# Performance work log

Measured on AMD Instinct MI355X. Metric: run time of the kernel, lower is better.

The kernel has to match this reference:

```python
import jax, jax.numpy as jnp
import numpy as np
import math

N, L, D = 1024, 32, 768
N_OUT, IN_DIM, OUT_DIM = 16, 64, 64
EPS = 1e-8


def setup_inputs() -> dict:
    key = jax.random.key(0)
    ks = jax.random.split(key, 4)
    x = jax.random.normal(ks[0], (N, L, D), jnp.float32)
    mask = jnp.ones((N, L), jnp.float32)
    scaled = lambda k, shape, fan: jax.random.normal(k, shape, jnp.float32) * (1.0 / np.sqrt(fan).astype(np.float32))
    Wscore = scaled(ks[1], (L, D, 1), D)
    Bscore = jnp.zeros((L, 1, 1), jnp.float32)
    Wcap = scaled(ks[2], (L, D, IN_DIM), D)
    Bcap = jnp.zeros((L, 1, IN_DIM), jnp.float32)
    Wvote = scaled(ks[3], (L, N_OUT, IN_DIM, OUT_DIM), IN_DIM)
    Bvote = jnp.zeros((L, N_OUT, 1, OUT_DIM), jnp.float32)
    beta_use = jnp.zeros((L, 1, 1, 1), jnp.float32)
    beta_ign = jnp.zeros((1, N_OUT, 1, 1), jnp.float32)
    return dict(x=x, mask=mask, Wscore=Wscore, Bscore=Bscore, Wcap=Wcap,
                Bcap=Bcap, Wvote=Wvote, Bvote=Bvote, beta_use=beta_use,
                beta_ign=beta_ign, iters=3)


def reference(x, mask, Wscore, Bscore, Wcap, Bcap, Wvote, Bvote, beta_use, beta_ign, iters):
    n_out = Wvote.shape[1]
    half_pi = np.float32(0.5 * math.pi)
    x_t = jnp.transpose(x, (1, 0, 2))                      # [L, N, D]
    a_in = jnp.matmul(x_t, Wscore) + Bscore                # [L, N, 1]
    mu_in = jax.nn.gelu(jnp.matmul(x_t, Wcap) + Bcap, approximate=False)  # [L, N, in_dim]
    f_a_in = jax.nn.sigmoid(a_in) * jnp.transpose(mask)[..., None]        # [L, N, 1]
    f_a_in = f_a_in[:, None, :, :]                         # [L, 1, N, 1]
    # votes: [L, n_out, N, out_dim] (einsum avoids materializing repeated mu_in)
    V = jnp.einsum('lni,lkio->lkno', mu_in, Wvote) + Bvote

    R = jnp.full((1, n_out, 1, 1), 1.0 / n_out, dtype=x.dtype)
    a_out = mu_out = var_out = None
    for t in range(iters):
        if t > 0:
            log_p = (-jnp.sum((V - mu_out[None]) ** 2 / (2.0 * var_out[None] + EPS), axis=-1)
                     - 1.0 - half_pi
                     - 0.5 * jnp.sum(jnp.log(var_out[None] + EPS), axis=-1))   # [L, n_out, N]
            R = jax.nn.softmax(jax.nn.log_sigmoid(a_out)[None] + log_p[..., None], axis=1)
        D_use = f_a_in * R                                  # [L, n_out, N, 1]
        D_ign = f_a_in - D_use
        a_out = jnp.sum(beta_use * D_use, axis=0) - jnp.sum(beta_ign * D_ign, axis=0)  # [n_out, N, 1]
        denom = jnp.sum(D_use, axis=0) + EPS                # [n_out, N, 1]
        mu_out = jnp.sum(D_use * V, axis=0) / denom         # [n_out, N, out_dim]
        var_out = jnp.sum(D_use * (V - mu_out[None]) ** 2, axis=0) / denom

    a_fin = jnp.transpose(a_out[..., 0])                    # [N, n_out]
    mu_fin = jnp.transpose(mu_out, (1, 0, 2))               # [N, n_out, out_dim]
    return a_fin, mu_fin
```

## Files before the change

### kernel.cpp

```cpp
#include <hip/hip_runtime.h>
#include <hip/hip_bf16.h>

#define L_DIM 32
#define N_DIM 1024
#define D_DIM 768
#define K_DIM 16
#define I_DIM 64
#define O_DIM 64
#define EPSF 1e-8f
#define PX 72

typedef unsigned short u16;
typedef __attribute__((ext_vector_type(8))) short short8;
typedef __attribute__((ext_vector_type(4))) float f32x4;
#define MFMA __builtin_amdgcn_mfma_f32_16x16x32_bf16

__device__ __forceinline__ float bf2f(u16 v) {
    union { unsigned int u; float f; } x; x.u = ((unsigned int)v) << 16; return x.f;
}
__device__ __forceinline__ u16 f2bf(float f) {
    union { float f; unsigned int u; } x; x.f = f;
    unsigned int u = x.u;
    u += 0x7FFFu + ((u >> 16) & 1u);
    return (u16)(u >> 16);
}
__device__ __forceinline__ void split2(float v, u16& h, u16& l) {
    u16 hh = f2bf(v);
    h = hh;
    l = f2bf(v - bf2f(hh));
}
__device__ __forceinline__ void store_split4(u16* ph, u16* pl, float4 v) {
    unsigned u0 = __float_as_uint(v.x), u1 = __float_as_uint(v.y);
    unsigned u2 = __float_as_uint(v.z), u3 = __float_as_uint(v.w);
    uint2 H, L;
    H.x = (u0 >> 16) | (u1 & 0xFFFF0000u);
    H.y = (u2 >> 16) | (u3 & 0xFFFF0000u);
    float l0 = v.x - __uint_as_float(u0 & 0xFFFF0000u);
    float l1 = v.y - __uint_as_float(u1 & 0xFFFF0000u);
    float l2 = v.z - __uint_as_float(u2 & 0xFFFF0000u);
    float l3 = v.w - __uint_as_float(u3 & 0xFFFF0000u);
    L.x = (__float_as_uint(l0) >> 16) | (__float_as_uint(l1) & 0xFFFF0000u);
    L.y = (__float_as_uint(l2) >> 16) | (__float_as_uint(l3) & 0xFFFF0000u);
    *(uint2*)ph = H;
    *(uint2*)pl = L;
}

__global__ __launch_bounds__(256) void prep_wcap(
    const float* __restrict__ W, u16* __restrict__ H, u16* __restrict__ Lo)
{
    const int l = blockIdx.y, d0 = blockIdx.x * 64, t = threadIdx.x;
    __shared__ float tile[64][65];
    #pragma unroll
    for (int p = 0; p < 4; p++) {
        int dd = p * 16 + (t >> 4), i4 = (t & 15) * 4;
        float4 v = *(const float4*)&W[((size_t)l * D_DIM + d0 + dd) * I_DIM + i4];
        tile[dd][i4] = v.x; tile[dd][i4+1] = v.y; tile[dd][i4+2] = v.z; tile[dd][i4+3] = v.w;
    }
    __syncthreads();
    #pragma unroll
    for (int p = 0; p < 4; p++) {
        int i = p * 16 + (t >> 4), dd0 = (t & 15) * 4;
        u16 h[4], lo[4];
        #pragma unroll
        for (int j = 0; j < 4; j++) split2(tile[dd0 + j][i], h[j], lo[j]);
        size_t base = ((size_t)l * I_DIM + i) * D_DIM + d0 + dd0;
        uint2 ph; ph.x = h[0] | ((unsigned)h[1] << 16); ph.y = h[2] | ((unsigned)h[3] << 16);
        uint2 pl; pl.x = lo[0] | ((unsigned)lo[1] << 16); pl.y = lo[2] | ((unsigned)lo[3] << 16);
        *(uint2*)&H[base] = ph;
        *(uint2*)&Lo[base] = pl;
    }
}

__global__ __launch_bounds__(256) void prep_wvote(
    const float* __restrict__ W, u16* __restrict__ H, u16* __restrict__ Lo)
{
    const int l = blockIdx.y, k = blockIdx.x, t = threadIdx.x;
    __shared__ float tile[64][65];
    #pragma unroll
    for (int p = 0; p < 4; p++) {
        int i = p * 16 + (t >> 4), o4 = (t & 15) * 4;
        float4 v = *(const float4*)&W[(((size_t)l * K_DIM + k) * I_DIM + i) * O_DIM + o4];
        tile[i][o4] = v.x; tile[i][o4+1] = v.y; tile[i][o4+2] = v.z; tile[i][o4+3] = v.w;
    }
    __syncthreads();
    #pragma unroll
    for (int p = 0; p < 4; p++) {
        int o = p * 16 + (t >> 4), i0 = (t & 15) * 4;
        u16 h[4], lo[4];
        #pragma unroll
        for (int j = 0; j < 4; j++) split2(tile[i0 + j][o], h[j], lo[j]);
        size_t base = (((size_t)l * K_DIM + k) * O_DIM + o) * I_DIM + i0;
        uint2 ph; ph.x = h[0] | ((unsigned)h[1] << 16); ph.y = h[2] | ((unsigned)h[3] << 16);
        uint2 pl; pl.x = lo[0] | ((unsigned)lo[1] << 16); pl.y = lo[2] | ((unsigned)lo[3] << 16);
        *(uint2*)&H[base] = ph;
        *(uint2*)&Lo[base] = pl;
    }
}

__global__ __launch_bounds__(256) void kernelA(
    const float* __restrict__ x, const float* __restrict__ mask,
    const float* __restrict__ Wscore, const float* __restrict__ Bscore,
    const u16* __restrict__ WcH, const u16* __restrict__ WcL,
    const float* __restrict__ Bcap,
    float* __restrict__ mu_out, float* __restrict__ fa_out,
    int nbase, int nchunk)
{
    const int l   = blockIdx.y;
    const int n0l = blockIdx.x * 32;
    const int t    = threadIdx.x;
    const int w    = t >> 6;
    const int lane = t & 63;
    const int quad = lane >> 4;
    const int ln16 = lane & 15;

    __shared__ u16 xh[2][32][PX], xl[2][32][PX];
    __shared__ float wsc_s[D_DIM];
    __shared__ float bcap_s[64];

    for (int i = t; i < D_DIM; i += 256) wsc_s[i] = Wscore[l * D_DIM + i];
    if (t < 64) bcap_s[t] = Bcap[l * I_DIM + t];

    const int sg = t >> 4;
    const int sd = (t & 15) * 4;

    const size_t xoff0 = ((size_t)(nbase + n0l + sg) * L_DIM + l) * D_DIM;
    const size_t xoff1 = ((size_t)(nbase + n0l + 16 + sg) * L_DIM + l) * D_DIM;

    float4 r0 = *(const float4*)&x[xoff0 + sd];
    float4 r1 = *(const float4*)&x[xoff1 + sd];

    __syncthreads();

    f32x4 acc[2] = {{0.f,0.f,0.f,0.f},{0.f,0.f,0.f,0.f}};
    float fa0 = 0.f, fa1 = 0.f;

    for (int ch = 0; ch < 12; ch++) {
        const int buf = ch & 1;
        const int k0 = ch * 64;

        {
            const float* wp = &wsc_s[k0 + sd];
            fa0 += r0.x * wp[0] + r0.y * wp[1] + r0.z * wp[2] + r0.w * wp[3];
            fa1 += r1.x * wp[0] + r1.y * wp[1] + r1.z * wp[2] + r1.w * wp[3];
        }
        store_split4(&xh[buf][sg][sd],      &xl[buf][sg][sd],      r0);
        store_split4(&xh[buf][16 + sg][sd], &xl[buf][16 + sg][sd], r1);
        __syncthreads();

        if (ch + 1 < 12) {
            const int k1 = k0 + 64;
            r0 = *(const float4*)&x[xoff0 + k1 + sd];
            r1 = *(const float4*)&x[xoff1 + k1 + sd];
        }

        #pragma unroll
        for (int ks = 0; ks < 2; ks++) {
            const int kk = ks * 32;
            size_t wbase = ((size_t)l * I_DIM + (w * 16 + ln16)) * D_DIM + k0 + kk + quad * 8;
            short8 ah = *(const short8*)&WcH[wbase];
            short8 al = *(const short8*)&WcL[wbase];
            #pragma unroll
            for (int c = 0; c < 2; c++) {
                const int n = c * 16 + ln16;
                short8 bh = *(const short8*)&xh[buf][n][kk + quad * 8];
                short8 bl = *(const short8*)&xl[buf][n][kk + quad * 8];
                acc[c] = MFMA(ah, bh, acc[c], 0, 0, 0);
                acc[c] = MFMA(ah, bl, acc[c], 0, 0, 0);
                acc[c] = MFMA(al, bh, acc[c], 0, 0, 0);
            }
        }
    }

    fa0 += __shfl_xor(fa0, 1, 64); fa1 += __shfl_xor(fa1, 1, 64);
    fa0 += __shfl_xor(fa0, 2, 64); fa1 += __shfl_xor(fa1, 2, 64);
    fa0 += __shfl_xor(fa0, 4, 64); fa1 += __shfl_xor(fa1, 4, 64);
    fa0 += __shfl_xor(fa0, 8, 64); fa1 += __shfl_xor(fa1, 8, 64);
    if ((t & 15) == 0) {
        float bs = Bscore[l];
        {
            float a = fa0 + bs;
            float sig = 1.f / (1.f + expf(-a));
            float m = mask[(size_t)(nbase + n0l + sg) * L_DIM + l];
            fa_out[(size_t)l * nchunk + n0l + sg] = sig * m;
        }
        {
            float a = fa1 + bs;
            float sig = 1.f / (1.f + expf(-a));
            float m = mask[(size_t)(nbase + n0l + 16 + sg) * L_DIM + l];
            fa_out[(size_t)l * nchunk + n0l + 16 + sg] = sig * m;
        }
    }

    #pragma unroll
    for (int c = 0; c < 2; c++) {
        const int n = c * 16 + ln16;
        const int i0 = w * 16 + quad * 4;
        float4 o;
        float* op = (float*)&o;
        #pragma unroll
        for (int r = 0; r < 4; r++) {
            float v = acc[c][r] + bcap_s[i0 + r];
            op[r] = 0.5f * v * (1.f + erff(v * 0.70710678118f));
        }
        *(float4*)&mu_out[((size_t)l * nchunk + n0l + n) * I_DIM + i0] = o;
    }
}

__global__ __launch_bounds__(256) void kernelB(
    const float* __restrict__ mu_in,
    const u16* __restrict__ WvH, const u16* __restrict__ WvL,
    const float* __restrict__ Bvote,
    float* __restrict__ V, int nchunk)
{
    const int l   = blockIdx.z;
    const int k   = blockIdx.y;
    const int n0l = blockIdx.x * 64;
    const int t    = threadIdx.x;
    const int w    = t >> 6;
    const int lane = t & 63;
    const int quad = lane >> 4;
    const int ln16 = lane & 15;

    __shared__ u16 mh[64][PX], ml[64][PX];
    __shared__ float bvote_s[64];

    if (t < 64) bvote_s[t] = Bvote[((size_t)l * K_DIM + k) * O_DIM + t];

    #pragma unroll
    for (int p = 0; p < 4; p++) {
        int n = p * 16 + (t >> 4), i0 = (t & 15) * 4;
        float4 v = *(const float4*)&mu_in[((size_t)l * nchunk + n0l + n) * I_DIM + i0];
        store_split4(&mh[n][i0], &ml[n][i0], v);
    }
    __syncthreads();

    f32x4 acc[4] = {{0.f,0.f,0.f,0.f},{0.f,0.f,0.f,0.f},{0.f,0.f,0.f,0.f},{0.f,0.f,0.f,0.f}};

    #pragma unroll
    for (int ks = 0; ks < 2; ks++) {
        const int kk = ks * 32;
        size_t wbase = (((size_t)l * K_DIM + k) * O_DIM + (w * 16 + ln16)) * I_DIM + kk + quad * 8;
        short8 ah = *(const short8*)&WvH[wbase];
        short8 al = *(const short8*)&WvL[wbase];
        #pragma unroll
        for (int c = 0; c < 4; c++) {
            const int n = c * 16 + ln16;
            short8 bh = *(const short8*)&mh[n][kk + quad * 8];
            short8 bl = *(const short8*)&ml[n][kk + quad * 8];
            acc[c] = MFMA(ah, bh, acc[c], 0, 0, 0);
            acc[c] = MFMA(ah, bl, acc[c], 0, 0, 0);
            acc[c] = MFMA(al, bh, acc[c], 0, 0, 0);
        }
    }

    #pragma unroll
    for (int c = 0; c < 4; c++) {
        const int n = c * 16 + ln16;
        const int o0 = w * 16 + quad * 4;
        float4 o;
        o.x = acc[c][0] + bvote_s[o0];
        o.y = acc[c][1] + bvote_s[o0 + 1];
        o.z = acc[c][2] + bvote_s[o0 + 2];
        o.w = acc[c][3] + bvote_s[o0 + 3];
        *(float4*)&V[(((size_t)l * K_DIM + k) * nchunk + n0l + n) * O_DIM + o0] = o;
    }
}

__global__ __launch_bounds__(256) void kernelC(
    const float* __restrict__ V, const float* __restrict__ fa_in,
    const float* __restrict__ beta_use, const float* __restrict__ beta_ign,
    const int* __restrict__ iters_p,
    float* __restrict__ out, int nbase, int nchunk)
{
    const int nl = blockIdx.x;
    const int ng = nbase + nl;
    const int t  = threadIdx.x;
    const int k  = t >> 4;
    const int og = (t & 15) << 2;
    int iters = iters_p[0];
    if (iters < 0 || iters > 16) iters = 3;

    __shared__ float fa_s[32];
    __shared__ float bu_s[32];
    __shared__ float R_s[32][17];
    __shared__ float sc_s[32][17];

    if (t < 32) {
        fa_s[t] = fa_in[(size_t)t * nchunk + nl];
        bu_s[t] = beta_use[t];
    }
    for (int idx = t; idx < 512; idx += 256)
        R_s[idx >> 4][idx & 15] = 1.f / 16.f;
    const float bi_k = beta_ign[k];

    float Vr[32][4];
    #pragma unroll
    for (int l = 0; l < 32; l++) {
        float4 v = *(const float4*)&V[(((size_t)l * K_DIM + k) * nchunk + nl) * O_DIM + og];
        Vr[l][0] = v.x; Vr[l][1] = v.y; Vr[l][2] = v.z; Vr[l][3] = v.w;
    }
    __syncthreads();

    float mu_r[4] = {0.f, 0.f, 0.f, 0.f};
    float var_r[4] = {0.f, 0.f, 0.f, 0.f};
    float a_r = 0.f;

    for (int it = 0; it < iters; it++) {
        if (it > 0) {
            float inv2v[4], lvp = 0.f;
            #pragma unroll
            for (int j = 0; j < 4; j++) {
                inv2v[j] = 1.f / (2.f * var_r[j] + EPSF);
                lvp += logf(var_r[j] + EPSF);
            }
            lvp += __shfl_xor(lvp, 1, 64);
            lvp += __shfl_xor(lvp, 2, 64);
            lvp += __shfl_xor(lvp, 4, 64);
            lvp += __shfl_xor(lvp, 8, 64);
            float ls = fminf(a_r, 0.f) - log1pf(expf(-fabsf(a_r)));
            const float cst = ls - 1.f - 1.57079632679f - 0.5f * lvp;
            #pragma unroll
            for (int l = 0; l < 32; l++) {
                float s = 0.f;
                #pragma unroll
                for (int j = 0; j < 4; j++) {
                    float d = Vr[l][j] - mu_r[j];
                    s += d * d * inv2v[j];
                }
                s = -s;
                s += __shfl_xor(s, 1, 64);
                s += __shfl_xor(s, 2, 64);
                s += __shfl_xor(s, 4, 64);
                s += __shfl_xor(s, 8, 64);
                if ((t & 15) == 0) sc_s[l][k] = s + cst;
            }
            __syncthreads();
            {
                const int lr = t >> 3;
                const int c2 = (t & 7) * 2;
                float s0 = sc_s[lr][c2], s1 = sc_s[lr][c2 + 1];
                float m = fmaxf(s0, s1);
                m = fmaxf(m, __shfl_xor(m, 1, 64));
                m = fmaxf(m, __shfl_xor(m, 2, 64));
                m = fmaxf(m, __shfl_xor(m, 4, 64));
                float e0 = expf(s0 - m), e1 = expf(s1 - m);
                float sum = e0 + e1;
                sum += __shfl_xor(sum, 1, 64);
                sum += __shfl_xor(sum, 2, 64);
                sum += __shfl_xor(sum, 4, 64);
                float inv = 1.f / sum;
                R_s[lr][c2]     = e0 * inv;
                R_s[lr][c2 + 1] = e1 * inv;
            }
            __syncthreads();
        }
        float denom = EPSF, a_acc = 0.f;
        float mu_a[4] = {0.f, 0.f, 0.f, 0.f};
        float v2_a[4] = {0.f, 0.f, 0.f, 0.f};
        #pragma unroll
        for (int l = 0; l < 32; l++) {
            float Du = fa_s[l] * R_s[l][k];
            denom += Du;
            a_acc += bu_s[l] * Du - bi_k * (fa_s[l] - Du);
            #pragma unroll
            for (int j = 0; j < 4; j++) {
                float dv = Du * Vr[l][j];
                mu_a[j] += dv;
                v2_a[j] += dv * Vr[l][j];
            }
        }
        float invd = 1.f / denom;
        #pragma unroll
        for (int j = 0; j < 4; j++) {
            mu_r[j] = mu_a[j] * invd;
            var_r[j] = fmaxf(v2_a[j] * invd - mu_r[j] * mu_r[j], 0.f);
        }
        a_r = a_acc;
    }

    if ((t & 15) == 0) out[(size_t)ng * K_DIM + k] = a_r;
    float4 o4;
    o4.x = mu_r[0]; o4.y = mu_r[1]; o4.z = mu_r[2]; o4.w = mu_r[3];
    *(float4*)&out[(size_t)N_DIM * K_DIM + ((size_t)ng * K_DIM + k) * O_DIM + og] = o4;
}

extern "C" void kernel_launch(void* const* d_in, const int* in_sizes, int n_in,
                              void* d_out, int out_size, void* d_ws, size_t ws_size,
                              hipStream_t stream) {
    (void)out_size;
    static const int EXP[11] = {25165824, 32768, 24576, 32, 1572864, 64,
                                2097152, 65536, 32, 16, 1};
    int mapi[11];
    bool used[64] = {false};
    for (int s = 0; s < 11; s++) {
        mapi[s] = (s < n_in) ? s : 0;
        for (int j = 0; j < n_in && j < 64; j++) {
            if (!used[j] && in_sizes[j] == EXP[s]) { mapi[s] = j; used[j] = true; break; }
        }
    }
    const float* x        = (const float*)d_in[mapi[0]];
    const float* mask     = (const float*)d_in[mapi[1]];
    const float* Wscore   = (const float*)d_in[mapi[2]];
    const float* Bscore   = (const float*)d_in[mapi[3]];
    const float* Wcap     = (const float*)d_in[mapi[4]];
    const float* Bcap     = (const float*)d_in[mapi[5]];
    const float* Wvote    = (const float*)d_in[mapi[6]];
    const float* Bvote    = (const float*)d_in[mapi[7]];
    const float* beta_use = (const float*)d_in[mapi[8]];
    const float* beta_ign = (const float*)d_in[mapi[9]];
    const int*   iters    = (const int*)d_in[mapi[10]];
    float* out = (float*)d_out;

    const size_t WCAP = (size_t)L_DIM * I_DIM * D_DIM;
    const size_t WVOT = (size_t)L_DIM * K_DIM * O_DIM * I_DIM;
    const size_t WBYTES = 2 * WCAP * 2 + 2 * WVOT * 2;

    int C = 64;
    {
        const int cands[5] = {1024, 512, 256, 128, 64};
        for (int i = 0; i < 5; i++) {
            size_t need = WBYTES + (size_t)cands[i] * (128 + 8192 + 131072);
            if (need <= ws_size) { C = cands[i]; break; }
        }
    }

    char* ws = (char*)d_ws;
    u16* WcH = (u16*)ws;
    u16* WcL = (u16*)(ws + WCAP * 2);
    u16* WvH = (u16*)(ws + WCAP * 4);
    u16* WvL = (u16*)(ws + WCAP * 4 + WVOT * 2);
    char* dyn = ws + WBYTES;
    float* fa = (float*)dyn;
    float* mu = (float*)(dyn + (size_t)128 * C);
    float* V  = (float*)(dyn + (size_t)128 * C + (size_t)8192 * C);

    prep_wcap<<<dim3(12, 32), 256, 0, stream>>>(Wcap, WcH, WcL);
    prep_wvote<<<dim3(16, 32), 256, 0, stream>>>(Wvote, WvH, WvL);

    for (int nbase = 0; nbase < N_DIM; nbase += C) {
        kernelA<<<dim3(C / 32, 32), 256, 0, stream>>>(
            x, mask, Wscore, Bscore, WcH, WcL, Bcap, mu, fa, nbase, C);
        kernelB<<<dim3(C / 64, 16, 32), 256, 0, stream>>>(
            mu, WvH, WvL, Bvote, V, C);
        kernelC<<<dim3(C), 256, 0, stream>>>(
            V, fa, beta_use, beta_ign, iters, out, nbase, C);
    }
}
```

Baseline: 296.8 us.

## Prefetch weights into registers and remap block indices for XCD locality

kernelA is fully unrolled with two register-resident prefetch stages: x and the Wcap hi/lo fragments are loaded one chunk ahead, so global latency overlaps the MFMA work. kernelB hoists its Wvote fragment and mu_in loads before the shared-memory split and the bias load. Both kernels remap the linear block id so consecutive blocks, which are spread across the 8 XCDs, share a layer l and keep its weights in a single XCD's L2. This raises register pressure, and kernelA now declares launch bounds of 256 threads with 4 blocks per CU.

```diff
diff --git a/kernel.cpp b/kernel.cpp
--- a/kernel.cpp
+++ b/kernel.cpp
@@ -97,7 +97,51 @@
     }
 }
 
-__global__ __launch_bounds__(256) void kernelA(
+
+#define A_CHUNK(K0, R0, R1, WH0, WL0, WH1, WL1, BUF)                        \
+  {                                                                          \
+    const float* wp = &wsc_s[(K0) + sd];                                     \
+    fa0 += R0.x * wp[0] + R0.y * wp[1] + R0.z * wp[2] + R0.w * wp[3];        \
+    fa1 += R1.x * wp[0] + R1.y * wp[1] + R1.z * wp[2] + R1.w * wp[3];        \
+    store_split4(&xh[BUF][sg][sd],      &xl[BUF][sg][sd],      R0);          \
+    store_split4(&xh[BUF][16 + sg][sd], &xl[BUF][16 + sg][sd], R1);          \
+    __syncthreads();                                                         \
+    if ((K0) + 128 < D_DIM) {                                                \
+      R0 = *(const float4*)&x[xoff0 + (K0) + 128 + sd];                      \
+      R1 = *(const float4*)&x[xoff1 + (K0) + 128 + sd];                      \
+    }                                                                        \
+    {                                                                        \
+      short8 bh, bl;                                                         \
+      bh = *(const short8*)&xh[BUF][ln16][quad * 8];                         \
+      bl = *(const short8*)&xl[BUF][ln16][quad * 8];                         \
+      acc0 = MFMA(WH0, bh, acc0, 0, 0, 0);                                   \
+      acc0 = MFMA(WH0, bl, acc0, 0, 0, 0);                                   \
+      acc0 = MFMA(WL0, bh, acc0, 0, 0, 0);                                   \
+      bh = *(const short8*)&xh[BUF][16 + ln16][quad * 8];                    \
+      bl = *(const short8*)&xl[BUF][16 + ln16][quad * 8];                    \
+      acc1 = MFMA(WH0, bh, acc1, 0, 0, 0);                                   \
+      acc1 = MFMA(WH0, bl, acc1, 0, 0, 0);                                   \
+      acc1 = MFMA(WL0, bh, acc1, 0, 0, 0);                                   \
+      bh = *(const short8*)&xh[BUF][ln16][32 + quad * 8];                    \
+      bl = *(const short8*)&xl[BUF][ln16][32 + quad * 8];                    \
+      acc0 = MFMA(WH1, bh, acc0, 0, 0, 0);                                   \
+      acc0 = MFMA(WH1, bl, acc0, 0, 0, 0);                                   \
+      acc0 = MFMA(WL1, bh, acc0, 0, 0, 0);                                   \
+      bh = *(const short8*)&xh[BUF][16 + ln16][32 + quad * 8];               \
+      bl = *(const short8*)&xl[BUF][16 + ln16][32 + quad * 8];               \
+      acc1 = MFMA(WH1, bh, acc1, 0, 0, 0);                                   \
+      acc1 = MFMA(WH1, bl, acc1, 0, 0, 0);                                   \
+      acc1 = MFMA(WL1, bh, acc1, 0, 0, 0);                                   \
+    }                                                                        \
+    if ((K0) + 128 < D_DIM) {                                                \
+      WH0 = *(const short8*)&WcH[wrow + (K0) + 128];                         \
+      WL0 = *(const short8*)&WcL[wrow + (K0) + 128];                         \
+      WH1 = *(const short8*)&WcH[wrow + (K0) + 160];                         \
+      WL1 = *(const short8*)&WcL[wrow + (K0) + 160];                         \
+    }                                                                        \
+  }
+
+__global__ __launch_bounds__(256, 4) void kernelA(
     const float* __restrict__ x, const float* __restrict__ mask,
     const float* __restrict__ Wscore, const float* __restrict__ Bscore,
     const u16* __restrict__ WcH, const u16* __restrict__ WcL,
@@ -105,8 +149,11 @@
     float* __restrict__ mu_out, float* __restrict__ fa_out,
     int nbase, int nchunk)
 {
-    const int l   = blockIdx.y;
-    const int n0l = blockIdx.x * 32;
+    const int bid  = blockIdx.y * gridDim.x + blockIdx.x;
+    const int slot = bid >> 3;
+    const int l    = (bid & 7) + 8 * (slot & 3);
+    const int n0l  = (slot >> 2) * 32;
+
     const int t    = threadIdx.x;
     const int w    = t >> 6;
     const int lane = t & 63;
@@ -126,49 +173,31 @@
     const size_t xoff0 = ((size_t)(nbase + n0l + sg) * L_DIM + l) * D_DIM;
     const size_t xoff1 = ((size_t)(nbase + n0l + 16 + sg) * L_DIM + l) * D_DIM;
 
-    float4 r0 = *(const float4*)&x[xoff0 + sd];
-    float4 r1 = *(const float4*)&x[xoff1 + sd];
+    float4 r0a = *(const float4*)&x[xoff0 + sd];
+    float4 r1a = *(const float4*)&x[xoff1 + sd];
+    float4 r0b = *(const float4*)&x[xoff0 + 64 + sd];
+    float4 r1b = *(const float4*)&x[xoff1 + 64 + sd];
+
+    const size_t wrow = ((size_t)l * I_DIM + (w * 16 + ln16)) * D_DIM + quad * 8;
+    short8 wha0 = *(const short8*)&WcH[wrow];
+    short8 wla0 = *(const short8*)&WcL[wrow];
+    short8 wha1 = *(const short8*)&WcH[wrow + 32];
+    short8 wla1 = *(const short8*)&WcL[wrow + 32];
+    short8 whb0 = *(const short8*)&WcH[wrow + 64];
+    short8 wlb0 = *(const short8*)&WcL[wrow + 64];
+    short8 whb1 = *(const short8*)&WcH[wrow + 96];
+    short8 wlb1 = *(const short8*)&WcL[wrow + 96];
 
     __syncthreads();
 
-    f32x4 acc[2] = {{0.f,0.f,0.f,0.f},{0.f,0.f,0.f,0.f}};
+    f32x4 acc0 = {0.f, 0.f, 0.f, 0.f};
+    f32x4 acc1 = {0.f, 0.f, 0.f, 0.f};
     float fa0 = 0.f, fa1 = 0.f;
 
-    for (int ch = 0; ch < 12; ch++) {
-        const int buf = ch & 1;
-        const int k0 = ch * 64;
-
-        {
-            const float* wp = &wsc_s[k0 + sd];
-            fa0 += r0.x * wp[0] + r0.y * wp[1] + r0.z * wp[2] + r0.w * wp[3];
-            fa1 += r1.x * wp[0] + r1.y * wp[1] + r1.z * wp[2] + r1.w * wp[3];
-        }
-        store_split4(&xh[buf][sg][sd],      &xl[buf][sg][sd],      r0);
-        store_split4(&xh[buf][16 + sg][sd], &xl[buf][16 + sg][sd], r1);
-        __syncthreads();
-
-        if (ch + 1 < 12) {
-            const int k1 = k0 + 64;
-            r0 = *(const float4*)&x[xoff0 + k1 + sd];
-            r1 = *(const float4*)&x[xoff1 + k1 + sd];
-        }
-
-        #pragma unroll
-        for (int ks = 0; ks < 2; ks++) {
-            const int kk = ks * 32;
-            size_t wbase = ((size_t)l * I_DIM + (w * 16 + ln16)) * D_DIM + k0 + kk + quad * 8;
-            short8 ah = *(const short8*)&WcH[wbase];
-            short8 al = *(const short8*)&WcL[wbase];
-            #pragma unroll
-            for (int c = 0; c < 2; c++) {
-                const int n = c * 16 + ln16;
-                short8 bh = *(const short8*)&xh[buf][n][kk + quad * 8];
-                short8 bl = *(const short8*)&xl[buf][n][kk + quad * 8];
-                acc[c] = MFMA(ah, bh, acc[c], 0, 0, 0);
-                acc[c] = MFMA(ah, bl, acc[c], 0, 0, 0);
-                acc[c] = MFMA(al, bh, acc[c], 0, 0, 0);
-            }
-        }
+    #pragma unroll
+    for (int cc = 0; cc < 6; cc++) {
+        A_CHUNK(cc * 128,      r0a, r1a, wha0, wla0, wha1, wla1, 0)
+        A_CHUNK(cc * 128 + 64, r0b, r1b, whb0, wlb0, whb1, wlb1, 1)
     }
 
     fa0 += __shfl_xor(fa0, 1, 64); fa1 += __shfl_xor(fa1, 1, 64);
@@ -193,13 +222,14 @@
 
     #pragma unroll
     for (int c = 0; c < 2; c++) {
+        const f32x4 a = (c == 0) ? acc0 : acc1;
         const int n = c * 16 + ln16;
         const int i0 = w * 16 + quad * 4;
         float4 o;
         float* op = (float*)&o;
         #pragma unroll
         for (int r = 0; r < 4; r++) {
-            float v = acc[c][r] + bcap_s[i0 + r];
+            float v = a[r] + bcap_s[i0 + r];
             op[r] = 0.5f * v * (1.f + erff(v * 0.70710678118f));
         }
         *(float4*)&mu_out[((size_t)l * nchunk + n0l + n) * I_DIM + i0] = o;
@@ -212,9 +242,13 @@
     const float* __restrict__ Bvote,
     float* __restrict__ V, int nchunk)
 {
-    const int l   = blockIdx.z;
-    const int k   = blockIdx.y;
-    const int n0l = blockIdx.x * 64;
+    const int bid  = (blockIdx.z * gridDim.y + blockIdx.y) * gridDim.x + blockIdx.x;
+    const int slot = bid >> 3;
+    const int l    = (bid & 7) + 8 * (slot & 3);
+    const int rem  = slot >> 2;
+    const int k    = rem & 15;
+    const int n0l  = (rem >> 4) * 64;
+
     const int t    = threadIdx.x;
     const int w    = t >> 6;
     const int lane = t & 63;
@@ -224,33 +258,45 @@
     __shared__ u16 mh[64][PX], ml[64][PX];
     __shared__ float bvote_s[64];
 
+    const int srow = t >> 4, scol = (t & 15) * 4;
+    float4 m0 = *(const float4*)&mu_in[((size_t)l * nchunk + n0l + srow) * I_DIM + scol];
+    float4 m1 = *(const float4*)&mu_in[((size_t)l * nchunk + n0l + 16 + srow) * I_DIM + scol];
+    float4 m2 = *(const float4*)&mu_in[((size_t)l * nchunk + n0l + 32 + srow) * I_DIM + scol];
+    float4 m3 = *(const float4*)&mu_in[((size_t)l * nchunk + n0l + 48 + srow) * I_DIM + scol];
+
+    const size_t wrow = (((size_t)l * K_DIM + k) * O_DIM + (w * 16 + ln16)) * I_DIM + quad * 8;
+    short8 ah0 = *(const short8*)&WvH[wrow];
+    short8 al0 = *(const short8*)&WvL[wrow];
+    short8 ah1 = *(const short8*)&WvH[wrow + 32];
+    short8 al1 = *(const short8*)&WvL[wrow + 32];
+
     if (t < 64) bvote_s[t] = Bvote[((size_t)l * K_DIM + k) * O_DIM + t];
 
-    #pragma unroll
-    for (int p = 0; p < 4; p++) {
-        int n = p * 16 + (t >> 4), i0 = (t & 15) * 4;
-        float4 v = *(const float4*)&mu_in[((size_t)l * nchunk + n0l + n) * I_DIM + i0];
-        store_split4(&mh[n][i0], &ml[n][i0], v);
-    }
+    store_split4(&mh[srow][scol],      &ml[srow][scol],      m0);
+    store_split4(&mh[16 + srow][scol], &ml[16 + srow][scol], m1);
+    store_split4(&mh[32 + srow][scol], &ml[32 + srow][scol], m2);
+    store_split4(&mh[48 + srow][scol], &ml[48 + srow][scol], m3);
     __syncthreads();
 
     f32x4 acc[4] = {{0.f,0.f,0.f,0.f},{0.f,0.f,0.f,0.f},{0.f,0.f,0.f,0.f},{0.f,0.f,0.f,0.f}};
 
     #pragma unroll
-    for (int ks = 0; ks < 2; ks++) {
-        const int kk = ks * 32;
-        size_t wbase = (((size_t)l * K_DIM + k) * O_DIM + (w * 16 + ln16)) * I_DIM + kk + quad * 8;
-        short8 ah = *(const short8*)&WvH[wbase];
-        short8 al = *(const short8*)&WvL[wbase];
-        #pragma unroll
-        for (int c = 0; c < 4; c++) {
-            const int n = c * 16 + ln16;
-            short8 bh = *(const short8*)&mh[n][kk + quad * 8];
-            short8 bl = *(const short8*)&ml[n][kk + quad * 8];
-            acc[c] = MFMA(ah, bh, acc[c], 0, 0, 0);
-            acc[c] = MFMA(ah, bl, acc[c], 0, 0, 0);
-            acc[c] = MFMA(al, bh, acc[c], 0, 0, 0);
-        }
+    for (int c = 0; c < 4; c++) {
+        const int n = c * 16 + ln16;
+        short8 bh = *(const short8*)&mh[n][quad * 8];
+        short8 bl = *(const short8*)&ml[n][quad * 8];
+        acc[c] = MFMA(ah0, bh, acc[c], 0, 0, 0);
+        acc[c] = MFMA(ah0, bl, acc[c], 0, 0, 0);
+        acc[c] = MFMA(al0, bh, acc[c], 0, 0, 0);
+    }
+    #pragma unroll
+    for (int c = 0; c < 4; c++) {
+        const int n = c * 16 + ln16;
+        short8 bh = *(const short8*)&mh[n][32 + quad * 8];
+        short8 bl = *(const short8*)&ml[n][32 + quad * 8];
+        acc[c] = MFMA(ah1, bh, acc[c], 0, 0, 0);
+        acc[c] = MFMA(ah1, bl, acc[c], 0, 0, 0);
+        acc[c] = MFMA(al1, bh, acc[c], 0, 0, 0);
     }
 
     #pragma unroll
```

After: 274.0 us. 7.7% less time.
